# Performance work log

Hardware: AMD Instinct MI355X
Metric: run time of the kernel (lower is better)

Reference implementation:

```python
import jax, jax.numpy as jnp
import numpy as np

DIM = 4096      # number of independent subUnits
SUB = 2         # sub_dim: width of each unit's slice
BATCH = 8192


def setup_inputs() -> dict:
    key = jax.random.key(0)
    kx, k1, k2 = jax.random.split(key, 3)
    x = jax.random.normal(kx, (BATCH, DIM * SUB), dtype=jnp.float32)
    # Per-unit weights for the two Linear(SUB, SUB, bias=False) layers,
    # stored as (in, out) so y = x @ W.
    W1 = jax.random.normal(k1, (DIM, SUB, SUB), dtype=jnp.float32) * 0.5
    W2 = jax.random.normal(k2, (DIM, SUB, SUB), dtype=jnp.float32) * 0.5
    return {"x": x, "W1": W1, "W2": W2}


def reference(x, W1, W2):
    B, TI = x.shape
    dim, sub, _ = W1.shape
    xu = x.reshape(B, dim, sub)                      # [B, dim, sub] slices
    h = jnp.einsum('bud,udh->buh', xu, W1)           # first linear per unit
    o = jnp.einsum('buh,uho->buo', h, W2)            # second linear per unit
    p = jax.nn.softmax(o, axis=-1)                   # softmax over sub dim
    oh = jax.nn.one_hot(jnp.argmax(p, axis=-1), sub, dtype=x.dtype)
    return oh.reshape(B, TI)
```

## Files before the change

### kernel.cpp

```cpp
#include <hip/hip_runtime.h>


#define BATCH 8192
#define DIMU  4096
#define NX    (BATCH * (size_t)DIMU * 2)
#define TOT_F4 ((size_t)BATCH * (size_t)(DIMU / 2))

__device__ __forceinline__ void unit_onehot(float x0, float x1,
                                            float4 w1, float4 w2,
                                            float& e0, float& e1) {
    const float h0 = __fadd_rn(__fmul_rn(x0, w1.x), __fmul_rn(x1, w1.z));
    const float h1 = __fadd_rn(__fmul_rn(x0, w1.y), __fmul_rn(x1, w1.w));
    const float o0 = __fadd_rn(__fmul_rn(h0, w2.x), __fmul_rn(h1, w2.z));
    const float o1 = __fadd_rn(__fmul_rn(h0, w2.y), __fmul_rn(h1, w2.w));
    const float t  = __fsub_rn(o1, o0);
    const bool one = (t > 0.0f) && (__fsub_rn(1.0f, t) < 1.0f);
    e0 = one ? 0.0f : 1.0f;
    e1 = one ? 1.0f : 0.0f;
}

__global__ __launch_bounds__(256) void onehot_units_kernel(
    const float* __restrict__ x,
    const float* __restrict__ W1,
    const float* __restrict__ W2,
    float* __restrict__ out)
{
    const size_t stride = (size_t)gridDim.x * blockDim.x;
    const float4* __restrict__ x4   = reinterpret_cast<const float4*>(x);
    const float4* __restrict__ w1_4 = reinterpret_cast<const float4*>(W1);
    const float4* __restrict__ w2_4 = reinterpret_cast<const float4*>(W2);
    float4* __restrict__ out4 = reinterpret_cast<float4*>(out);

    for (size_t i = (size_t)blockIdx.x * blockDim.x + threadIdx.x;
         i < TOT_F4; i += stride) {
        const float4 xv = x4[i];
        const int u = ((int)(i & (size_t)(DIMU / 2 - 1))) * 2;
        const float4 w1a = w1_4[u];
        const float4 w1b = w1_4[u + 1];
        const float4 w2a = w2_4[u];
        const float4 w2b = w2_4[u + 1];

        float4 ov;
        unit_onehot(xv.x, xv.y, w1a, w2a, ov.x, ov.y);
        unit_onehot(xv.z, xv.w, w1b, w2b, ov.z, ov.w);
        out4[i] = ov;
    }
}

extern "C" void kernel_launch(void* const* d_in, const int* in_sizes, int n_in,
                              void* d_out, int out_size, void* d_ws, size_t ws_size,
                              hipStream_t stream) {
    const float* x  = (const float*)d_in[0];
    const float* W1 = (const float*)d_in[1];
    const float* W2 = (const float*)d_in[2];
    if (n_in >= 3) {
        int xi = -1;
        for (int k = 0; k < 3; ++k) if (in_sizes[k] == (int)NX) xi = k;
        if (xi >= 0) {
            int wi = -1, wj = -1;
            for (int k = 0; k < 3; ++k) if (k != xi) { if (wi < 0) wi = k; else wj = k; }
            x  = (const float*)d_in[xi];
            W1 = (const float*)d_in[wi];
            W2 = (const float*)d_in[wj];
        }
    }
    float* out = (float*)d_out;

    dim3 grid(2048), block(256);
    hipLaunchKernelGGL(onehot_units_kernel, grid, block, 0, stream,
                       x, W1, W2, out);
}
```

Measured before the change: 129.6 us.

## Hoist per-unit weights into registers and loop each thread over 32 rows

Each thread now owns one unit pair and processes 32 batch rows, loading its W1/W2 float4s once instead of once per element. This cuts redundant weight loads (mostly cache hits) and index arithmetic. The grid-stride loop becomes a fixed-size loop with a grid sized exactly to the data, giving 2048 blocks with a partially unrolled inner loop. Memory traffic for x and out is unchanged, so the kernel stays bandwidth-bound.

New measurement: 115.3 us. 11.0% less time.

```diff
diff --git a/kernel.cpp b/kernel.cpp
--- a/kernel.cpp
+++ b/kernel.cpp
@@ -3,8 +3,10 @@
 
 #define BATCH 8192
 #define DIMU  4096
-#define NX    (BATCH * (size_t)DIMU * 2)
-#define TOT_F4 ((size_t)BATCH * (size_t)(DIMU / 2))
+#define NPAIR (DIMU / 2)
+#define NX    ((size_t)BATCH * DIMU * 2)
+#define NTHREADS ((size_t)BATCH * NPAIR / 32)
+#define ROWS  32
 
 __device__ __forceinline__ void unit_onehot(float x0, float x1,
                                             float4 w1, float4 w2,
@@ -25,25 +27,29 @@
     const float* __restrict__ W2,
     float* __restrict__ out)
 {
-    const size_t stride = (size_t)gridDim.x * blockDim.x;
+    const unsigned gid = blockIdx.x * blockDim.x + threadIdx.x;
+    const unsigned p     = gid & (NPAIR - 1);
+    const unsigned chunk = gid >> 11;
+    const unsigned r0    = chunk * ROWS;
+
     const float4* __restrict__ x4   = reinterpret_cast<const float4*>(x);
     const float4* __restrict__ w1_4 = reinterpret_cast<const float4*>(W1);
     const float4* __restrict__ w2_4 = reinterpret_cast<const float4*>(W2);
     float4* __restrict__ out4 = reinterpret_cast<float4*>(out);
 
-    for (size_t i = (size_t)blockIdx.x * blockDim.x + threadIdx.x;
-         i < TOT_F4; i += stride) {
-        const float4 xv = x4[i];
-        const int u = ((int)(i & (size_t)(DIMU / 2 - 1))) * 2;
-        const float4 w1a = w1_4[u];
-        const float4 w1b = w1_4[u + 1];
-        const float4 w2a = w2_4[u];
-        const float4 w2b = w2_4[u + 1];
+    const float4 w1a = w1_4[2 * p];
+    const float4 w1b = w1_4[2 * p + 1];
+    const float4 w2a = w2_4[2 * p];
+    const float4 w2b = w2_4[2 * p + 1];
 
+    size_t idx = (size_t)r0 * NPAIR + p;
+    #pragma unroll 4
+    for (int k = 0; k < ROWS; ++k, idx += NPAIR) {
+        const float4 xv = x4[idx];
         float4 ov;
         unit_onehot(xv.x, xv.y, w1a, w2a, ov.x, ov.y);
         unit_onehot(xv.z, xv.w, w1b, w2b, ov.z, ov.w);
-        out4[i] = ov;
+        out4[idx] = ov;
     }
 }
 
@@ -66,7 +72,7 @@
     }
     float* out = (float*)d_out;
 
-    dim3 grid(2048), block(256);
+    dim3 grid((unsigned)(NTHREADS / 256)), block(256);
     hipLaunchKernelGGL(onehot_units_kernel, grid, block, 0, stream,
                        x, W1, W2, out);
 }
```
